# Kernel optimization log

Measured on AMD Instinct MI355X. Metric: run time of the kernel, lower is better.

## Reference

```python
import jax, jax.numpy as jnp
import numpy as np

B = 30          # bandwidth
L = B           # degrees l = 0..L-1
NB = 2 * B      # spatial grid size per angle (beta/alpha/gamma)
MW = 2 * L - 1  # centered frequency index width, m in [-(L-1), L-1]
P = 6           # kernel grid points (n_alpha=6, n_beta=1)


def _wigner_d_all(betas, L):
    """Wigner-d matrices d^l_{m,n}(beta) via d^l(beta)=expm(-(beta/2)(J+ - J-)).
    Returns [len(betas), L, MW, MW], zero-padded for |m|,|n|>l."""
    betas = np.asarray(betas, dtype=np.float64)
    D = np.zeros((len(betas), L, MW, MW), dtype=np.float64)
    for l in range(L):
        dim = 2 * l + 1
        m = np.arange(-l, l)
        cp = np.sqrt(l * (l + 1) - m * (m + 1))  # <m+1|J+|m>
        A = np.zeros((dim, dim))
        A[np.arange(1, dim), np.arange(dim - 1)] = cp
        A = A - A.T  # J+ - J-, real antisymmetric
        lam, V = np.linalg.eigh(1j * A)  # Hermitian
        ph = np.exp(0.5j * betas[:, None] * lam[None, :])  # [nb, dim]
        dl = np.einsum('ab,jb,cb->jac', V, ph, V.conj()).real
        off = L - 1 - l
        D[:, l, off:off + dim, off:off + dim] = dl
    return D


def _s3_quadrature(b):
    """SOFT-grid quadrature weights over beta (lie_learn S3 formula, up to a constant)."""
    j = np.arange(2 * b)
    k = np.arange(b)[None, :]
    s = (np.sin(np.pi * (2 * j[:, None] + 1) * (2 * k + 1) / (4 * b)) / (2 * k + 1)).sum(axis=1)
    return (2.0 / b) * np.sin(np.pi * (2 * j + 1) / (4 * b)) * s


# ---- precomputed constants ----
_betas_sig = np.pi * (2 * np.arange(NB) + 1) / (4 * B)  # SOFT beta grid
_D_np = _wigner_d_all(_betas_sig, L)                    # [NB, L, MW, MW]
_alphas_k = np.linspace(0.0, 2.0 * np.pi, P, endpoint=False)
_Dk_np = _wigner_d_all(np.full(P, np.pi / 160.0), L)[:, :, :, L - 1]  # [P, L, MW], n=0 column
_idx_c = (np.arange(MW) - (L - 1)) % NB                 # centered m -> FFT bin
_nidx = np.arange(MW) - (L - 1)

D_SIG = jnp.asarray(_D_np, dtype=jnp.float32)
D0_SIG = jnp.asarray(_D_np[:, :, :, L - 1], dtype=jnp.float32)
D_KER = jnp.asarray(_Dk_np, dtype=jnp.float32)
W_QUAD = jnp.asarray(_s3_quadrature(B), dtype=jnp.float32)
FAC_L = jnp.asarray(2 * np.arange(L) + 1, dtype=jnp.float32)
E_KER = jnp.asarray(np.exp(-1j * _nidx[None, :] * _alphas_k[:, None]), dtype=jnp.complex64)


def s2_conv(x, wk):
    """FFT-based S2 convolution: S2 analysis -> spectral multiply -> SO(3) synthesis.
    x: [batch, f_in, NB(beta), NB(alpha)] real; wk: [f_in, f_out, P].
    Returns [batch, f_out, NB(beta), NB(alpha), NB(gamma)] real."""
    xf = jnp.fft.fft(x, axis=-1) * (2.0 * np.pi / NB)        # alpha -> m, complex64
    xfc = xf[..., _idx_c]                                     # centered m: [b,f,NB,MW]
    # S2 analysis: X^l_m = sum_beta w(beta) d^l_{m0}(beta) xhat(beta, m)
    X = jnp.einsum('j,jlm,bfjm->bflm', W_QUAD, D0_SIG, xfc)   # [b,f_in,L,MW]
    # kernel spectrum psi^l_n = sum_p wk_p d^l_{n0}(beta_p) e^{-i n alpha_p}
    psi = jnp.einsum('iop,pln,pn->ioln', wk.astype(jnp.complex64),
                     D_KER.astype(jnp.complex64), E_KER)      # [f_in,f_out,L,MW]
    # spectral mm: Z^l_{mn} = sum_{f_in} X^l_m conj(psi^l_n)
    Z = jnp.einsum('bilm,ioln->bolmn', X, jnp.conj(psi))      # [b,f_out,L,MW,MW]
    # SO(3) synthesis per beta: F(beta,m,n) = sum_l (2l+1) d^l_{mn}(beta) Z^l_{mn}
    F = jnp.einsum('l,jlmn,bolmn->bojmn', FAC_L, D_SIG, Z)    # [b,f_out,NB,MW,MW]
    G = jnp.zeros(F.shape[:3] + (NB, NB), dtype=F.dtype)
    G = G.at[..., _idx_c[:, None], _idx_c[None, :]].set(F)    # embed centered freqs
    return jnp.fft.ifft2(G, axes=(-2, -1)).real * float(NB * NB)


def so3_integrate_gamma(x):
    # matches the given so3_integrate: contracts ONLY the last (gamma) axis with w
    return jnp.einsum('...g,g->...', x, W_QUAD)


def setup_inputs() -> dict:
    key = jax.random.key(0)
    k1, k2, k3 = jax.random.split(key, 3)
    batch = 16
    x1 = jax.random.normal(k1, (batch, 2, NB, NB), dtype=jnp.float32)
    w_conv = jax.random.normal(k2, (2, 10, P), dtype=jnp.float32) / np.sqrt(2 * P)
    w_deconv = jax.random.normal(k3, (10, 2, P), dtype=jnp.float32) / np.sqrt(10 * P)
    return {"x1": x1, "w_conv": w_conv, "w_deconv": w_deconv}


def reference(x1, w_conv, w_deconv):
    x = s2_conv(x1, w_conv)        # encode: [b,10,60,60,60]
    x = so3_integrate_gamma(x)     # [b,10,60,60] (S2 signal)
    x = s2_conv(x, w_deconv)       # decode: [b,2,60,60,60]
    return so3_integrate_gamma(x)  # [b,2,60,60]
```

## Files before the change

### kernel.cpp

```cpp
#include <hip/hip_runtime.h>
#include <hip/hip_fp16.h>

#define NBG   60
#define LMAX  30
#define MWC   59
#define CTR   29
#define NPAIR 20
#define NT    11
#define NTP   12
#define NOFF  5
#define PI_F  3.14159265358979323846f

__device__ void wigner_colf(float beta, int mp, int mn, float scale,
                            float* out, int stride) {
  int a = mp - mn; if (a < 0) a = -a;
  int b = mp + mn; if (b < 0) b = -b;
  int lmin = (a + b) >> 1;
  for (int l = 0; l < LMAX; ++l) out[l * stride] = 0.0f;
  if (lmin >= LMAX) return;
  float sh, ch; sincosf(0.5f * beta, &sh, &ch);
  float x = ch * ch - sh * sh;
  float base = scale;
  for (int q = 0; q < a; ++q) base *= sh;
  for (int q = 0; q < b; ++q) base *= ch;
  if (mp >= mn && ((mp - mn) & 1)) base = -base;
  float K2 = 1.f;
  for (int q = 1; q <= a; ++q) K2 *= (float)(b + q) / (float)q;
  float Pm2 = 0.f, Pm1 = 1.f;
  out[lmin * stride] = base * sqrtf(K2);
  for (int s = 1; lmin + s < LMAX; ++s) {
    float Ps;
    if (s == 1) {
      Ps = (a + 1) + (a + b + 2) * 0.5f * (x - 1.f);
    } else {
      float t0 = 2.f * s + a + b;
      float c1 = 2.f * s * (s + a + b) * (t0 - 2.f);
      float c2 = (t0 - 1.f) * (t0 * (t0 - 2.f) * x + (float)(a * a - b * b));
      float c3 = 2.f * (s + a - 1.f) * (s + b - 1.f) * t0;
      Ps = (c2 * Pm1 - c3 * Pm2) / c1;
    }
    K2 *= ((float)s * (s + a + b)) / (((float)s + a) * ((float)s + b));
    out[(lmin + s) * stride] = base * sqrtf(K2) * Ps;
    Pm2 = Pm1; Pm1 = Ps;
  }
}

__device__ __forceinline__ float quad_w(int j) {
  float s = 0.f;
  for (int k = 0; k < 30; ++k) {
    int r = ((2 * j + 1) * (2 * k + 1)) % 240;
    s += sinf(2.f * PI_F * r / 240.f) / (float)(2 * k + 1);
  }
  return (2.f / 30.f) * sinf(PI_F * (2 * j + 1) / 120.f) * s;
}

__global__ __launch_bounds__(256)
void k1_prep(const float* __restrict__ x1,
             const float* __restrict__ wc, const float* __restrict__ wd,
             float2* __restrict__ scwF1, float2* __restrict__ scwF2,
             float* __restrict__ D0T, float* __restrict__ sgd,
             float2* __restrict__ xfT) {
  __shared__ __align__(16) char smem[23104];
  int bi = blockIdx.x, t = threadIdx.x;

  if (bi == 0) {
    float*  swq  = (float*)smem;
    float2* swqn = (float2*)(smem + 240);
    if (t < NBG) swq[t] = quad_w(t);
    __syncthreads();
    if (t < NT) {
      int n = t - NOFF;
      float re = 0.f, im = 0.f;
      for (int g = 0; g < NBG; ++g) {
        int k = ((n * g) % NBG + NBG) % NBG;
        float sn, cs; sincosf(2.f * PI_F * k / 60.f, &sn, &cs);
        re += swq[g] * cs; im += swq[g] * sn;
      }
      swqn[t] = make_float2(re, im);
    }
    __syncthreads();
    if (t < NT * NPAIR) {
      int nn = t / NPAIR, pair = t - nn * NPAIR, n = nn - NOFF;
      float re1 = 0, im1 = 0, re2 = 0, im2 = 0;
      for (int p = 0; p < 6; ++p) {
        int k = ((n * p) % 6 + 6) % 6;
        float sn, cs; sincosf(2.f * PI_F * k / 6.f, &sn, &cs);
        float a1 = wc[pair * 6 + p], a2 = wd[pair * 6 + p];
        re1 += a1 * cs; im1 += a1 * sn;
        re2 += a2 * cs; im2 += a2 * sn;
      }
      float2 w = swqn[nn];
      scwF1[t] = make_float2(w.x * re1 - w.y * im1, w.x * im1 + w.y * re1);
      scwF2[t] = make_float2(PI_F * (w.x * re2 - w.y * im2),
                             PI_F * (w.x * im2 + w.y * re2));
    }
  } else if (bi < 60) {
    int M = bi - 1;
    if (t < NBG) {
      float wqj = quad_w(t);
      wigner_colf(PI_F * (2 * t + 1) / 120.f, M - CTR, 0, wqj,
                  D0T + (size_t)M * LMAX * NBG + t, NBG);
    }
  } else if (bi < 180) {
    float* buf  = (float*)smem;
    float* dkwL = (float*)(smem + 21600);
    int s = bi - 60, j = s >> 1, Mq = s & 1;
    if (t < 15 * NT) {
      int Mi = t / NT, nn = t - Mi * NT;
      int mp = Mq * 15 + Mi - CTR, mn = nn - NOFF;
      wigner_colf(PI_F * (2 * j + 1) / 120.f, mp, mn, 1.f,
                  &buf[Mi * LMAX * NTP + nn], NTP);
    } else if (t >= 165 && t < 165 + NT) {
      int nn = t - 165;
      wigner_colf(PI_F / 160.f, nn - NOFF, 0, 1.f, dkwL + nn, NTP);
      for (int l = 0; l < LMAX; ++l) dkwL[l * NTP + nn] *= (float)(2 * l + 1);
    }
    __syncthreads();
    size_t base = (size_t)(j * 30 + Mq * 15) * LMAX * NTP;
    for (int q = t; q < 15 * LMAX * NTP; q += 256) {
      int r = q % (LMAX * NTP), l = r / NTP, nn = r - l * NTP;
      float v = (nn < NT) ? buf[q] * dkwL[l * NTP + nn] : 0.f;
      sgd[base + q] = v;
    }
  } else {
    float*  xr  = (float*)smem;
    float*  twc = (float*)(smem + 1920);
    float*  tws = (float*)(smem + 2160);
    float2* xo  = (float2*)(smem + 2400);
    int s = bi - 180, j = s >> 2, qh = s & 3;
    for (int q = t; q < 8 * NBG; q += 256) {
      int bl = q / NBG, a = q - bl * NBG;
      xr[bl * NBG + a] = x1[((size_t)(qh * 8 + bl) * NBG + j) * NBG + a];
    }
    if (t < NBG) {
      float sn, cs; sincosf(-2.f * PI_F * t / 60.f, &sn, &cs);
      twc[t] = cs; tws[t] = sn;
    }
    __syncthreads();
    for (int q = t; q < 8 * MWC; q += 256) {
      int bl = q / MWC, M = q - bl * MWC, mm = M - CTR;
      const float* xp = xr + bl * NBG;
      float re = 0.f, im = 0.f; int k = 0;
      for (int a = 0; a < NBG; ++a) {
        re += xp[a] * twc[k]; im += xp[a] * tws[k];
        k += mm; if (k >= NBG) k -= NBG; if (k < 0) k += NBG;
      }
      const float sc = 2.f * PI_F / 60.f;
      xo[M * 9 + bl] = make_float2(re * sc, im * sc);
    }
    __syncthreads();
    for (int q = t; q < MWC * 8; q += 256) {
      int M = q / 8, bl = q - M * 8;
      xfT[((size_t)M * NBG + j) * 32 + qh * 8 + bl] = xo[M * 9 + bl];
    }
  }
}

__global__ __launch_bounds__(256)
void k_ana1(const float2* __restrict__ xfT, const float* __restrict__ D0T,
            float2* __restrict__ X21) {
  __shared__ float2 sxf[NBG][32];
  __shared__ float  sD[8][NBG];
  int M = blockIdx.x >> 2, lq = blockIdx.x & 3;
  int t = threadIdx.x;
  for (int q = t; q < NBG * 32; q += 256) ((float2*)sxf)[q] = xfT[(size_t)M * NBG * 32 + q];
  for (int q = t; q < 8 * NBG; q += 256) {
    int ll = q / NBG, jj = q - ll * NBG, l = lq * 8 + ll;
    sD[ll][jj] = (l < LMAX) ? D0T[((size_t)M * LMAX + l) * NBG + jj] : 0.f;
  }
  __syncthreads();
  int ll = t >> 5, w = t & 31, i = w >> 4, b = w & 15;
  int l = lq * 8 + ll;
  if (l < LMAX) {
    float re = 0.f, im = 0.f;
#pragma unroll 6
    for (int jj = 0; jj < NBG; ++jj) {
      float d = sD[ll][jj];
      float2 v = sxf[jj][b * 2 + i];
      re += d * v.x; im += d * v.y;
    }
    X21[(size_t)M * LMAX * 32 + l * 32 + w] = make_float2(re, im);
  }
}

__global__ __launch_bounds__(256)
void k_core1(const float2* __restrict__ X2, const float* __restrict__ sgd,
             const float2* __restrict__ scwF, __half2* __restrict__ Th) {
  __shared__ float  sg[2][LMAX][NTP];
  __shared__ float2 scw[NT * NPAIR];
  __shared__ float2 sC[2][LMAX][NPAIR];
  __shared__ float2 sX[2][LMAX][32];
  int t = threadIdx.x;
  int j = blockIdx.x / 30, mg = blockIdx.x - 30 * j;
  int Mbase = mg * 2;

  for (int q = t; q < NT * NPAIR; q += 256) scw[q] = scwF[q];
  for (int q = t; q < 2 * LMAX * 32; q += 256) {
    int Mi = q / (LMAX * 32), r = q - Mi * (LMAX * 32);
    int M = Mbase + Mi;
    ((float2*)sX)[q] = (M < MWC) ? X2[(size_t)M * LMAX * 32 + r]
                                 : make_float2(0.f, 0.f);
  }
  for (int q = t; q < 2 * LMAX * NTP; q += 256) {
    int Mi = q / (LMAX * NTP), r = q - Mi * LMAX * NTP;
    int l = r / NTP, nn = r - l * NTP;
    int M = Mbase + Mi;
    float v = 0.f;
    if (M < MWC && nn < NT) {
      if (M < 30) {
        v = sgd[(size_t)(j * 30 + M) * LMAX * NTP + r];
      } else {
        v = sgd[(size_t)(j * 30 + 58 - M) * LMAX * NTP + l * NTP + (10 - nn)];
        if (!(M & 1)) v = -v;
      }
    }
    ((float*)sg)[q] = v;
  }
  __syncthreads();

  for (int q = t; q < 2 * LMAX * NPAIR; q += 256) {
    int Mi = q / (LMAX * NPAIR), r = q - Mi * LMAX * NPAIR;
    int l = r / NPAIR, pair = r - l * NPAIR;
    float cre = 0.f, cim = 0.f;
#pragma unroll
    for (int nn = 0; nn < NT; ++nn) {
      float g = sg[Mi][l][nn];
      float2 c = scw[nn * NPAIR + pair];
      cre += g * c.x; cim += g * c.y;
    }
    ((float2*)sC)[q] = make_float2(cre, cim);
  }
  __syncthreads();

  for (int q = t; q < 2 * 160; q += 256) {
    int Mi = q / 160, u = q - Mi * 160;
    int M = Mbase + Mi;
    if (M >= MWC) continue;
    int bb = u / 10, o = u - 10 * bb;
    float tre = 0.f, tim = 0.f;
#pragma unroll 6
    for (int l = 0; l < LMAX; ++l) {
#pragma unroll
      for (int i = 0; i < 2; ++i) {
        float2 xv = sX[Mi][l][i * 16 + bb];
        float2 cv = sC[Mi][l][i * 10 + o];
        tre += xv.x * cv.x - xv.y * cv.y;
        tim += xv.x * cv.y + xv.y * cv.x;
      }
    }
    Th[((size_t)j * MWC + M) * 160 + u] = __floats2half2_rn(tre, tim);
  }
}

__global__ __launch_bounds__(256)
void k_ana2(const __half2* __restrict__ T1, const float* __restrict__ D0T,
            float2* __restrict__ X22) {
  __shared__ float2 sxf[NBG][40];
  __shared__ float  sD[LMAX][NBG];
  int M = blockIdx.x >> 2, q4 = blockIdx.x & 3;
  int u0 = q4 * 40, t = threadIdx.x;
  for (int q = t; q < NBG * 40; q += 256) {
    int jj = q / 40, uq = q - jj * 40;
    float2 v1 = __half22float2(T1[((size_t)jj * MWC + M) * 160 + u0 + uq]);
    float2 v2 = __half22float2(T1[((size_t)jj * MWC + (58 - M)) * 160 + u0 + uq]);
    sxf[jj][uq] = make_float2(v1.x + v2.x, v1.y - v2.y);
  }
  for (int q = t; q < LMAX * NBG; q += 256) ((float*)sD)[q] = D0T[(size_t)M * LMAX * NBG + q];
  __syncthreads();
  for (int q = t; q < LMAX * 40; q += 256) {
    int l = q / 40, w = q - l * 40;
    float re = 0.f, im = 0.f;
#pragma unroll 6
    for (int jj = 0; jj < NBG; ++jj) {
      float d = sD[l][jj];
      float2 v = sxf[jj][w];
      re += d * v.x; im += d * v.y;
    }
    int uu = u0 + w;
    int p = (uu % 10) * 16 + uu / 10;
    X22[((size_t)M * LMAX + l) * 160 + p] = make_float2(re, im);
  }
}

__global__ __launch_bounds__(256)
void k_core2(const float2* __restrict__ X2, const float* __restrict__ sgd,
             const float2* __restrict__ scwF, float2* __restrict__ Tf) {
  __shared__ float  sg[2][LMAX][NTP];
  __shared__ float2 scw[NT * NPAIR];
  __shared__ float2 sC[2][LMAX][NPAIR];
  __shared__ float2 sRed[256];
  int t = threadIdx.x;
  int j = blockIdx.x / 30, mg = blockIdx.x - 30 * j;
  int Mbase = mg * 2;

  for (int q = t; q < NT * NPAIR; q += 256) scw[q] = scwF[q];
  for (int q = t; q < 2 * LMAX * NTP; q += 256) {
    int Mi = q / (LMAX * NTP), r = q - Mi * LMAX * NTP;
    int l = r / NTP, nn = r - l * NTP;
    int M = Mbase + Mi;
    float v = 0.f;
    if (M < MWC && nn < NT) {
      if (M < 30) {
        v = sgd[(size_t)(j * 30 + M) * LMAX * NTP + r];
      } else {
        v = sgd[(size_t)(j * 30 + 58 - M) * LMAX * NTP + l * NTP + (10 - nn)];
        if (!(M & 1)) v = -v;
      }
    }
    ((float*)sg)[q] = v;
  }
  __syncthreads();

  for (int q = t; q < 2 * LMAX * NPAIR; q += 256) {
    int Mi = q / (LMAX * NPAIR), r = q - Mi * LMAX * NPAIR;
    int l = r / NPAIR, pair = r - l * NPAIR;
    float cre = 0.f, cim = 0.f;
#pragma unroll
    for (int nn = 0; nn < NT; ++nn) {
      float g = sg[Mi][l][nn];
      float2 c = scw[nn * NPAIR + pair];
      cre += g * c.x; cim += g * c.y;
    }
    ((float2*)sC)[q] = make_float2(cre, cim);
  }
  __syncthreads();

  int sub = t >> 6, idx = t & 63;
  int Mi = idx >> 5, u = idx & 31;
  int M = Mbase + Mi;
  int bb = u >> 1, o = u & 1;
  float tre = 0.f, tim = 0.f;
  if (M < MWC) {
    for (int l = sub; l < LMAX; l += 4) {
#pragma unroll
      for (int i = 0; i < 10; ++i) {
        float2 xv = X2[((size_t)M * LMAX + l) * 160 + i * 16 + bb];
        float2 cv = sC[Mi][l][i * 2 + o];
        tre += xv.x * cv.x - xv.y * cv.y;
        tim += xv.x * cv.y + xv.y * cv.x;
      }
    }
  }
  sRed[t] = make_float2(tre, tim);
  __syncthreads();
  if (t < 64 && M < MWC) {
    float2 a0 = sRed[t], a1 = sRed[t + 64], a2 = sRed[t + 128], a3 = sRed[t + 192];
    Tf[((size_t)j * MWC + M) * 32 + u] =
        make_float2(a0.x + a1.x + a2.x + a3.x, a0.y + a1.y + a2.y + a3.y);
  }
}

__global__ __launch_bounds__(256)
void k_synth2(const float2* __restrict__ T2, float* __restrict__ out) {
  __shared__ float2 sT[MWC][16];
  __shared__ float twc[NBG], tws[NBG];
  int j = blockIdx.x >> 1, uh = blockIdx.x & 1;
  int u0 = uh * 16, t = threadIdx.x;
  for (int q = t; q < MWC * 16; q += 256) {
    int M = q / 16, uu = q - M * 16;
    sT[M][uu] = T2[((size_t)j * MWC + M) * 32 + u0 + uu];
  }
  if (t < NBG) {
    float s, c; sincosf(2.f * PI_F * t / 60.f, &s, &c);
    twc[t] = c; tws[t] = s;
  }
  __syncthreads();
  for (int q = t; q < 16 * NBG; q += 256) {
    int uu = q / NBG, a = q - uu * NBG;
    int k = (31 * a) % NBG;
    float acc = 0.f;
#pragma unroll 4
    for (int M = 0; M < MWC; ++M) {
      float2 v = sT[M][uu];
      acc += v.x * twc[k] - v.y * tws[k];
      k += a; if (k >= NBG) k -= NBG;
    }
    out[((size_t)(u0 + uu) * NBG + j) * NBG + a] = acc;
  }
}

extern "C" void kernel_launch(void* const* d_in, const int* in_sizes, int n_in,
                              void* d_out, int out_size, void* d_ws, size_t ws_size,
                              hipStream_t stream) {
  const float* x1       = (const float*)d_in[0];
  const float* w_conv   = (const float*)d_in[1];
  const float* w_deconv = (const float*)d_in[2];
  float* out = (float*)d_out;
  char* ws = (char*)d_ws;

  float2*  scwF1 = (float2*) (ws + 0);
  float2*  scwF2 = (float2*) (ws + 2048);
  float*   D0T   = (float*)  (ws + 4096);
  float*   sgd   = (float*)  (ws + 430080);
  char*    R1    = ws + 3022592;
  char*    R2    = ws + 5288192;
  float2*  X21   = (float2*) (ws + 7553792);
  float2*  xfT   = (float2*) R1;
  float2*  X22   = (float2*) R1;
  __half2* T1    = (__half2*)R2;
  float2*  T2    = (float2*) R2;

  k1_prep<<<420, 256, 0, stream>>>(x1, w_conv, w_deconv, scwF1, scwF2, D0T, sgd, xfT);
  k_ana1<<<236, 256, 0, stream>>>(xfT, D0T, X21);
  k_core1<<<1800, 256, 0, stream>>>(X21, sgd, scwF1, T1);
  k_ana2<<<236, 256, 0, stream>>>(T1, D0T, X22);
  k_core2<<<1800, 256, 0, stream>>>(X22, sgd, scwF2, T2);
  k_synth2<<<120, 256, 0, stream>>>(T2, out);
}
```

Measured before the change: 101.0 us.

## Fuse beta-analysis into core stages and re-split wigner prep blocks

Merges k_ana1 with k_core1 and k_ana2 with k_core2 into two fused kernels. Each block keeps its per-M Legendre-analysis result in shared memory (fp16 for the second stage) and then loops over ten beta rows, which removes the X21/X22 global round trips and two launches. The prep kernel's Wigner table build is split into more, smaller blocks. In exchange the fused kernels run only 180 blocks with large shared-memory footprints, and each block repeats the analysis work serially, which may cut parallelism and occupancy.

After: 203.0 us. 101% more time.

```diff
diff --git a/kernel.cpp b/kernel.cpp
--- a/kernel.cpp
+++ b/kernel.cpp
@@ -60,12 +60,11 @@
              float2* __restrict__ scwF1, float2* __restrict__ scwF2,
              float* __restrict__ D0T, float* __restrict__ sgd,
              float2* __restrict__ xfT) {
-  __shared__ __align__(16) char smem[23104];
-  int bi = blockIdx.x, t = threadIdx.x;
-
-  if (bi == 0) {
+  __shared__ __align__(16) char smem[13056];
+  int u = blockIdx.x, t = threadIdx.x;
+  if (u == 0) {
     float*  swq  = (float*)smem;
-    float2* swqn = (float2*)(smem + 240);
+    float2* swqn = (float2*)(smem + 256);
     if (t < NBG) swq[t] = quad_w(t);
     __syncthreads();
     if (t < NT) {
@@ -94,40 +93,39 @@
       scwF2[t] = make_float2(PI_F * (w.x * re2 - w.y * im2),
                              PI_F * (w.x * im2 + w.y * re2));
     }
-  } else if (bi < 60) {
-    int M = bi - 1;
+  } else if (u < 60) {
+    int M = u - 1;
     if (t < NBG) {
       float wqj = quad_w(t);
       wigner_colf(PI_F * (2 * t + 1) / 120.f, M - CTR, 0, wqj,
                   D0T + (size_t)M * LMAX * NBG + t, NBG);
     }
-  } else if (bi < 180) {
+  } else if (u < 300) {
     float* buf  = (float*)smem;
-    float* dkwL = (float*)(smem + 21600);
-    int s = bi - 60, j = s >> 1, Mq = s & 1;
-    if (t < 15 * NT) {
+    float* dkwL = (float*)(smem + 11520);
+    int s = u - 60, j = s >> 2, c = s & 3;
+    int M0 = c * 8, nM = (c < 3) ? 8 : 6;
+    if (t < nM * NT) {
       int Mi = t / NT, nn = t - Mi * NT;
-      int mp = Mq * 15 + Mi - CTR, mn = nn - NOFF;
-      wigner_colf(PI_F * (2 * j + 1) / 120.f, mp, mn, 1.f,
-                  &buf[Mi * LMAX * NTP + nn], NTP);
-    } else if (t >= 165 && t < 165 + NT) {
-      int nn = t - 165;
+      wigner_colf(PI_F * (2 * j + 1) / 120.f, M0 + Mi - CTR, nn - NOFF, 1.f,
+                  &buf[Mi * 360 + nn], NTP);
+    } else if (t >= 128 && t < 128 + NT) {
+      int nn = t - 128;
       wigner_colf(PI_F / 160.f, nn - NOFF, 0, 1.f, dkwL + nn, NTP);
       for (int l = 0; l < LMAX; ++l) dkwL[l * NTP + nn] *= (float)(2 * l + 1);
     }
     __syncthreads();
-    size_t base = (size_t)(j * 30 + Mq * 15) * LMAX * NTP;
-    for (int q = t; q < 15 * LMAX * NTP; q += 256) {
-      int r = q % (LMAX * NTP), l = r / NTP, nn = r - l * NTP;
-      float v = (nn < NT) ? buf[q] * dkwL[l * NTP + nn] : 0.f;
-      sgd[base + q] = v;
+    size_t base = (size_t)(j * 30 + M0) * 360;
+    for (int q = t; q < nM * 360; q += 256) {
+      int r = q % 360, nn = r % NTP;
+      sgd[base + q] = (nn < NT) ? buf[q] * dkwL[r] : 0.f;
     }
   } else {
     float*  xr  = (float*)smem;
     float*  twc = (float*)(smem + 1920);
     float*  tws = (float*)(smem + 2160);
     float2* xo  = (float2*)(smem + 2400);
-    int s = bi - 180, j = s >> 2, qh = s & 3;
+    int s = u - 300, j = s >> 2, qh = s & 3;
     for (int q = t; q < 8 * NBG; q += 256) {
       int bl = q / NBG, a = q - bl * NBG;
       xr[bl * NBG + a] = x1[((size_t)(qh * 8 + bl) * NBG + j) * NBG + a];
@@ -157,196 +155,202 @@
 }
 
 __global__ __launch_bounds__(256)
-void k_ana1(const float2* __restrict__ xfT, const float* __restrict__ D0T,
-            float2* __restrict__ X21) {
-  __shared__ float2 sxf[NBG][32];
-  __shared__ float  sD[8][NBG];
-  int M = blockIdx.x >> 2, lq = blockIdx.x & 3;
+void k_fused1(const float2* __restrict__ xfT, const float* __restrict__ D0T,
+              const float* __restrict__ sgd, const float2* __restrict__ scwF,
+              __half2* __restrict__ T1) {
+  __shared__ __align__(16) char smem[52160];
+  float2* sxf  = (float2*)smem;
+  float*  sD   = (float*)(smem + 15360);
+  float2* sX21 = (float2*)(smem + 22560);
+  float2* scw  = (float2*)(smem + 37920);
+  float*  sg   = (float*)(smem + 39680);
+  float2* sC   = (float2*)(smem + 42560);
   int t = threadIdx.x;
-  for (int q = t; q < NBG * 32; q += 256) ((float2*)sxf)[q] = xfT[(size_t)M * NBG * 32 + q];
-  for (int q = t; q < 8 * NBG; q += 256) {
-    int ll = q / NBG, jj = q - ll * NBG, l = lq * 8 + ll;
-    sD[ll][jj] = (l < LMAX) ? D0T[((size_t)M * LMAX + l) * NBG + jj] : 0.f;
+  int mg = blockIdx.x / 6, jq = blockIdx.x - 6 * mg;
+  int Mbase = mg * 2, j0 = jq * 10;
+  for (int q = t; q < NT * NPAIR; q += 256) scw[q] = scwF[q];
+  for (int Mi = 0; Mi < 2; ++Mi) {
+    int M = Mbase + Mi;
+    if (M < MWC) {
+      __syncthreads();
+      for (int q = t; q < NBG * 32; q += 256) sxf[q] = xfT[(size_t)M * NBG * 32 + q];
+      for (int q = t; q < LMAX * NBG; q += 256) sD[q] = D0T[(size_t)M * LMAX * NBG + q];
+      __syncthreads();
+      for (int q = t; q < 960; q += 256) {
+        int l = q >> 5, w = q & 31, i = w >> 4, b = w & 15;
+        float re = 0.f, im = 0.f;
+#pragma unroll 6
+        for (int j = 0; j < NBG; ++j) {
+          float d = sD[l * NBG + j];
+          float2 v = sxf[j * 32 + b * 2 + i];
+          re += d * v.x; im += d * v.y;
+        }
+        sX21[Mi * 960 + q] = make_float2(re, im);
+      }
+    } else {
+      for (int q = t; q < 960; q += 256) sX21[Mi * 960 + q] = make_float2(0.f, 0.f);
+    }
   }
   __syncthreads();
-  int ll = t >> 5, w = t & 31, i = w >> 4, b = w & 15;
-  int l = lq * 8 + ll;
-  if (l < LMAX) {
-    float re = 0.f, im = 0.f;
+  for (int jj = 0; jj < 10; ++jj) {
+    int j = j0 + jj;
+    for (int q = t; q < 720; q += 256) {
+      int Mi = q / 360, r = q - Mi * 360;
+      int l = r / NTP, nn = r - l * NTP;
+      int M = Mbase + Mi;
+      float v = 0.f;
+      if (M < MWC && nn < NT) {
+        if (M < 30) {
+          v = sgd[(size_t)(j * 30 + M) * 360 + r];
+        } else {
+          v = sgd[(size_t)(j * 30 + 58 - M) * 360 + l * NTP + (10 - nn)];
+          if (!(M & 1)) v = -v;
+        }
+      }
+      sg[q] = v;
+    }
+    __syncthreads();
+    for (int q = t; q < 1200; q += 256) {
+      int Mi = q / 600, r = q - Mi * 600;
+      int l = r / NPAIR, pair = r - l * NPAIR;
+      float cre = 0.f, cim = 0.f;
+#pragma unroll
+      for (int nn = 0; nn < NT; ++nn) {
+        float g = sg[Mi * 360 + l * NTP + nn];
+        float2 c = scw[nn * NPAIR + pair];
+        cre += g * c.x; cim += g * c.y;
+      }
+      sC[q] = make_float2(cre, cim);
+    }
+    __syncthreads();
+    for (int q = t; q < 320; q += 256) {
+      int Mi = q / 160, u = q - Mi * 160;
+      int M = Mbase + Mi;
+      if (M < MWC) {
+        int bb = u / 10, o = u - 10 * bb;
+        float tre = 0.f, tim = 0.f;
 #pragma unroll 6
-    for (int jj = 0; jj < NBG; ++jj) {
-      float d = sD[ll][jj];
-      float2 v = sxf[jj][b * 2 + i];
-      re += d * v.x; im += d * v.y;
-    }
-    X21[(size_t)M * LMAX * 32 + l * 32 + w] = make_float2(re, im);
+        for (int l = 0; l < LMAX; ++l) {
+#pragma unroll
+          for (int i = 0; i < 2; ++i) {
+            float2 xv = sX21[Mi * 960 + l * 32 + i * 16 + bb];
+            float2 cv = sC[Mi * 600 + l * NPAIR + i * 10 + o];
+            tre += xv.x * cv.x - xv.y * cv.y;
+            tim += xv.x * cv.y + xv.y * cv.x;
+          }
+        }
+        T1[((size_t)j * MWC + M) * 160 + u] = __floats2half2_rn(tre, tim);
+      }
+    }
+    __syncthreads();
   }
 }
 
 __global__ __launch_bounds__(256)
-void k_core1(const float2* __restrict__ X2, const float* __restrict__ sgd,
-             const float2* __restrict__ scwF, __half2* __restrict__ Th) {
-  __shared__ float  sg[2][LMAX][NTP];
-  __shared__ float2 scw[NT * NPAIR];
-  __shared__ float2 sC[2][LMAX][NPAIR];
-  __shared__ float2 sX[2][LMAX][32];
+void k_fused2(const __half2* __restrict__ T1, const float* __restrict__ D0T,
+              const float* __restrict__ sgd, const float2* __restrict__ scwF,
+              float2* __restrict__ T2) {
+  __shared__ __align__(16) char smem[60000];
+  __half2* sX22 = (__half2*)smem;
+  float*   sD   = (float*)(smem + 40800);
+  __half2* sxf  = (__half2*)(smem + 55200);
   int t = threadIdx.x;
-  int j = blockIdx.x / 30, mg = blockIdx.x - 30 * j;
-  int Mbase = mg * 2;
-
+  int mg = blockIdx.x / 6, jq = blockIdx.x - 6 * mg;
+  int Mbase = mg * 2, j0 = jq * 10;
+  for (int q = t; q < 2 * LMAX * NBG; q += 256) {
+    int Mi = q / (LMAX * NBG), r = q - Mi * LMAX * NBG;
+    int M = Mbase + Mi;
+    sD[q] = (M < MWC) ? D0T[(size_t)M * LMAX * NBG + r] : 0.f;
+  }
+  __syncthreads();
+  for (int c = 0; c < 8; ++c) {
+    int u0 = c * 20;
+    for (int Mi = 0; Mi < 2; ++Mi) {
+      int M = Mbase + Mi;
+      if (M >= MWC) continue;
+      for (int q = t; q < NBG * 20; q += 256) {
+        int j = q / 20, w = q - j * 20;
+        float2 v1 = __half22float2(T1[((size_t)j * MWC + M) * 160 + u0 + w]);
+        float2 v2 = __half22float2(T1[((size_t)j * MWC + (58 - M)) * 160 + u0 + w]);
+        sxf[q] = __floats2half2_rn(v1.x + v2.x, v1.y - v2.y);
+      }
+      __syncthreads();
+      for (int q = t; q < LMAX * 20; q += 256) {
+        int l = q / 20, w = q - l * 20;
+        float re = 0.f, im = 0.f;
+#pragma unroll 6
+        for (int j = 0; j < NBG; ++j) {
+          float d = sD[Mi * 1800 + l * NBG + j];
+          float2 v = __half22float2(sxf[j * 20 + w]);
+          re += d * v.x; im += d * v.y;
+        }
+        int uu = u0 + w;
+        int p = (uu % 10) * 17 + uu / 10;
+        sX22[Mi * 5100 + l * 170 + p] = __floats2half2_rn(re, im);
+      }
+      __syncthreads();
+    }
+  }
+  float2* scw  = (float2*)(smem + 40800);
+  float*  sg   = (float*)(smem + 42560);
+  float2* sC   = (float2*)(smem + 45440);
+  float2* sRed = (float2*)(smem + 55040);
   for (int q = t; q < NT * NPAIR; q += 256) scw[q] = scwF[q];
-  for (int q = t; q < 2 * LMAX * 32; q += 256) {
-    int Mi = q / (LMAX * 32), r = q - Mi * (LMAX * 32);
+  for (int jj = 0; jj < 10; ++jj) {
+    int j = j0 + jj;
+    for (int q = t; q < 720; q += 256) {
+      int Mi = q / 360, r = q - Mi * 360;
+      int l = r / NTP, nn = r - l * NTP;
+      int M = Mbase + Mi;
+      float v = 0.f;
+      if (M < MWC && nn < NT) {
+        if (M < 30) {
+          v = sgd[(size_t)(j * 30 + M) * 360 + r];
+        } else {
+          v = sgd[(size_t)(j * 30 + 58 - M) * 360 + l * NTP + (10 - nn)];
+          if (!(M & 1)) v = -v;
+        }
+      }
+      sg[q] = v;
+    }
+    __syncthreads();
+    for (int q = t; q < 1200; q += 256) {
+      int Mi = q / 600, r = q - Mi * 600;
+      int l = r / NPAIR, pair = r - l * NPAIR;
+      float cre = 0.f, cim = 0.f;
+#pragma unroll
+      for (int nn = 0; nn < NT; ++nn) {
+        float g = sg[Mi * 360 + l * NTP + nn];
+        float2 c = scw[nn * NPAIR + pair];
+        cre += g * c.x; cim += g * c.y;
+      }
+      sC[q] = make_float2(cre, cim);
+    }
+    __syncthreads();
+    int sub = t >> 6, idx = t & 63;
+    int Mi = idx >> 5, u = idx & 31;
     int M = Mbase + Mi;
-    ((float2*)sX)[q] = (M < MWC) ? X2[(size_t)M * LMAX * 32 + r]
-                                 : make_float2(0.f, 0.f);
-  }
-  for (int q = t; q < 2 * LMAX * NTP; q += 256) {
-    int Mi = q / (LMAX * NTP), r = q - Mi * LMAX * NTP;
-    int l = r / NTP, nn = r - l * NTP;
-    int M = Mbase + Mi;
-    float v = 0.f;
-    if (M < MWC && nn < NT) {
-      if (M < 30) {
-        v = sgd[(size_t)(j * 30 + M) * LMAX * NTP + r];
-      } else {
-        v = sgd[(size_t)(j * 30 + 58 - M) * LMAX * NTP + l * NTP + (10 - nn)];
-        if (!(M & 1)) v = -v;
-      }
-    }
-    ((float*)sg)[q] = v;
-  }
-  __syncthreads();
-
-  for (int q = t; q < 2 * LMAX * NPAIR; q += 256) {
-    int Mi = q / (LMAX * NPAIR), r = q - Mi * LMAX * NPAIR;
-    int l = r / NPAIR, pair = r - l * NPAIR;
-    float cre = 0.f, cim = 0.f;
+    int bb = u >> 1, o = u & 1;
+    float tre = 0.f, tim = 0.f;
+    if (M < MWC) {
+      for (int l = sub; l < LMAX; l += 4) {
 #pragma unroll
-    for (int nn = 0; nn < NT; ++nn) {
-      float g = sg[Mi][l][nn];
-      float2 c = scw[nn * NPAIR + pair];
-      cre += g * c.x; cim += g * c.y;
-    }
-    ((float2*)sC)[q] = make_float2(cre, cim);
-  }
-  __syncthreads();
-
-  for (int q = t; q < 2 * 160; q += 256) {
-    int Mi = q / 160, u = q - Mi * 160;
-    int M = Mbase + Mi;
-    if (M >= MWC) continue;
-    int bb = u / 10, o = u - 10 * bb;
-    float tre = 0.f, tim = 0.f;
-#pragma unroll 6
-    for (int l = 0; l < LMAX; ++l) {
-#pragma unroll
-      for (int i = 0; i < 2; ++i) {
-        float2 xv = sX[Mi][l][i * 16 + bb];
-        float2 cv = sC[Mi][l][i * 10 + o];
-        tre += xv.x * cv.x - xv.y * cv.y;
-        tim += xv.x * cv.y + xv.y * cv.x;
-      }
-    }
-    Th[((size_t)j * MWC + M) * 160 + u] = __floats2half2_rn(tre, tim);
-  }
-}
-
-__global__ __launch_bounds__(256)
-void k_ana2(const __half2* __restrict__ T1, const float* __restrict__ D0T,
-            float2* __restrict__ X22) {
-  __shared__ float2 sxf[NBG][40];
-  __shared__ float  sD[LMAX][NBG];
-  int M = blockIdx.x >> 2, q4 = blockIdx.x & 3;
-  int u0 = q4 * 40, t = threadIdx.x;
-  for (int q = t; q < NBG * 40; q += 256) {
-    int jj = q / 40, uq = q - jj * 40;
-    float2 v1 = __half22float2(T1[((size_t)jj * MWC + M) * 160 + u0 + uq]);
-    float2 v2 = __half22float2(T1[((size_t)jj * MWC + (58 - M)) * 160 + u0 + uq]);
-    sxf[jj][uq] = make_float2(v1.x + v2.x, v1.y - v2.y);
-  }
-  for (int q = t; q < LMAX * NBG; q += 256) ((float*)sD)[q] = D0T[(size_t)M * LMAX * NBG + q];
-  __syncthreads();
-  for (int q = t; q < LMAX * 40; q += 256) {
-    int l = q / 40, w = q - l * 40;
-    float re = 0.f, im = 0.f;
-#pragma unroll 6
-    for (int jj = 0; jj < NBG; ++jj) {
-      float d = sD[l][jj];
-      float2 v = sxf[jj][w];
-      re += d * v.x; im += d * v.y;
-    }
-    int uu = u0 + w;
-    int p = (uu % 10) * 16 + uu / 10;
-    X22[((size_t)M * LMAX + l) * 160 + p] = make_float2(re, im);
-  }
-}
-
-__global__ __launch_bounds__(256)
-void k_core2(const float2* __restrict__ X2, const float* __restrict__ sgd,
-             const float2* __restrict__ scwF, float2* __restrict__ Tf) {
-  __shared__ float  sg[2][LMAX][NTP];
-  __shared__ float2 scw[NT * NPAIR];
-  __shared__ float2 sC[2][LMAX][NPAIR];
-  __shared__ float2 sRed[256];
-  int t = threadIdx.x;
-  int j = blockIdx.x / 30, mg = blockIdx.x - 30 * j;
-  int Mbase = mg * 2;
-
-  for (int q = t; q < NT * NPAIR; q += 256) scw[q] = scwF[q];
-  for (int q = t; q < 2 * LMAX * NTP; q += 256) {
-    int Mi = q / (LMAX * NTP), r = q - Mi * LMAX * NTP;
-    int l = r / NTP, nn = r - l * NTP;
-    int M = Mbase + Mi;
-    float v = 0.f;
-    if (M < MWC && nn < NT) {
-      if (M < 30) {
-        v = sgd[(size_t)(j * 30 + M) * LMAX * NTP + r];
-      } else {
-        v = sgd[(size_t)(j * 30 + 58 - M) * LMAX * NTP + l * NTP + (10 - nn)];
-        if (!(M & 1)) v = -v;
-      }
-    }
-    ((float*)sg)[q] = v;
-  }
-  __syncthreads();
-
-  for (int q = t; q < 2 * LMAX * NPAIR; q += 256) {
-    int Mi = q / (LMAX * NPAIR), r = q - Mi * LMAX * NPAIR;
-    int l = r / NPAIR, pair = r - l * NPAIR;
-    float cre = 0.f, cim = 0.f;
-#pragma unroll
-    for (int nn = 0; nn < NT; ++nn) {
-      float g = sg[Mi][l][nn];
-      float2 c = scw[nn * NPAIR + pair];
-      cre += g * c.x; cim += g * c.y;
-    }
-    ((float2*)sC)[q] = make_float2(cre, cim);
-  }
-  __syncthreads();
-
-  int sub = t >> 6, idx = t & 63;
-  int Mi = idx >> 5, u = idx & 31;
-  int M = Mbase + Mi;
-  int bb = u >> 1, o = u & 1;
-  float tre = 0.f, tim = 0.f;
-  if (M < MWC) {
-    for (int l = sub; l < LMAX; l += 4) {
-#pragma unroll
-      for (int i = 0; i < 10; ++i) {
-        float2 xv = X2[((size_t)M * LMAX + l) * 160 + i * 16 + bb];
-        float2 cv = sC[Mi][l][i * 2 + o];
-        tre += xv.x * cv.x - xv.y * cv.y;
-        tim += xv.x * cv.y + xv.y * cv.x;
-      }
-    }
-  }
-  sRed[t] = make_float2(tre, tim);
-  __syncthreads();
-  if (t < 64 && M < MWC) {
-    float2 a0 = sRed[t], a1 = sRed[t + 64], a2 = sRed[t + 128], a3 = sRed[t + 192];
-    Tf[((size_t)j * MWC + M) * 32 + u] =
-        make_float2(a0.x + a1.x + a2.x + a3.x, a0.y + a1.y + a2.y + a3.y);
+        for (int i = 0; i < 10; ++i) {
+          float2 xv = __half22float2(sX22[Mi * 5100 + l * 170 + i * 17 + bb]);
+          float2 cv = sC[Mi * 600 + l * NPAIR + i * 2 + o];
+          tre += xv.x * cv.x - xv.y * cv.y;
+          tim += xv.x * cv.y + xv.y * cv.x;
+        }
+      }
+    }
+    sRed[t] = make_float2(tre, tim);
+    __syncthreads();
+    if (t < 64 && M < MWC) {
+      float2 a0 = sRed[t], a1 = sRed[t + 64], a2 = sRed[t + 128], a3 = sRed[t + 192];
+      T2[((size_t)j * MWC + M) * 32 + u] =
+          make_float2(a0.x + a1.x + a2.x + a3.x, a0.y + a1.y + a2.y + a3.y);
+    }
+    __syncthreads();
   }
 }
 
@@ -382,9 +386,9 @@
 extern "C" void kernel_launch(void* const* d_in, const int* in_sizes, int n_in,
                               void* d_out, int out_size, void* d_ws, size_t ws_size,
                               hipStream_t stream) {
-  const float* x1       = (const float*)d_in[0];
-  const float* w_conv   = (const float*)d_in[1];
-  const float* w_deconv = (const float*)d_in[2];
+  const float* x1 = (const float*)d_in[0];
+  const float* wc = (const float*)d_in[1];
+  const float* wd = (const float*)d_in[2];
   float* out = (float*)d_out;
   char* ws = (char*)d_ws;
 
@@ -392,18 +396,12 @@
   float2*  scwF2 = (float2*) (ws + 2048);
   float*   D0T   = (float*)  (ws + 4096);
   float*   sgd   = (float*)  (ws + 430080);
-  char*    R1    = ws + 3022592;
-  char*    R2    = ws + 5288192;
-  float2*  X21   = (float2*) (ws + 7553792);
-  float2*  xfT   = (float2*) R1;
-  float2*  X22   = (float2*) R1;
-  __half2* T1    = (__half2*)R2;
-  float2*  T2    = (float2*) R2;
-
-  k1_prep<<<420, 256, 0, stream>>>(x1, w_conv, w_deconv, scwF1, scwF2, D0T, sgd, xfT);
-  k_ana1<<<236, 256, 0, stream>>>(xfT, D0T, X21);
-  k_core1<<<1800, 256, 0, stream>>>(X21, sgd, scwF1, T1);
-  k_ana2<<<236, 256, 0, stream>>>(T1, D0T, X22);
-  k_core2<<<1800, 256, 0, stream>>>(X22, sgd, scwF2, T2);
+  float2*  xfT   = (float2*) (ws + 3022592);
+  __half2* T1    = (__half2*)(ws + 3929088);
+  float2*  T2    = (float2*) (ws + 6194944);
+
+  k1_prep <<<540, 256, 0, stream>>>(x1, wc, wd, scwF1, scwF2, D0T, sgd, xfT);
+  k_fused1<<<180, 256, 0, stream>>>(xfT, D0T, sgd, scwF1, T1);
+  k_fused2<<<180, 256, 0, stream>>>(T1, D0T, sgd, scwF2, T2);
   k_synth2<<<120, 256, 0, stream>>>(T2, out);
 }
```
